# Kernel tuning notes

Hardware: AMD Instinct MI355X
Metric: run time of the kernel (lower is better)

Reference implementation:

```python
import jax, jax.numpy as jnp
import numpy as np

X, Y, Z, E, K, ITERS = 128, 128, 8, 64, 3, 3
XYZ = X * Y * Z
IMG_H, IMG_W = 384, 1280
FH, FW = 96, 320  # img_feat spatial size
LN_EPS = 1e-5
GRAD_SCALE = 0.1


def _homo_grid():
    # get_coordinates: meshgrid(arange(x), -arange(y), arange(z)), then append ones
    xs = (np.arange(X) * 0.8 + 0.0).astype(np.float32)
    ys = (-(np.arange(Y) * 0.8 - 51.2)).astype(np.float32)
    zs = (np.arange(Z) * 0.5 - 2.5).astype(np.float32)
    gx, gy, gz = np.meshgrid(xs, ys, zs, indexing='ij')
    g = np.stack([gx, gy, gz, np.ones_like(gx)], axis=-1)  # (X,Y,Z,4)
    return jnp.asarray(g)


def _grid_sample(img, grid):
    # F.grid_sample: bilinear, padding_mode='zeros', align_corners=False
    # img: (B,C,H,W), grid: (B,N,K,2) xy in [-1,1] -> out (B,C,N,K)
    B, C, H, W = img.shape
    x = ((grid[..., 0] + 1.0) * W - 1.0) * 0.5
    y = ((grid[..., 1] + 1.0) * H - 1.0) * 0.5
    x0 = jnp.floor(x); y0 = jnp.floor(y)
    x1 = x0 + 1.0; y1 = y0 + 1.0
    wx1 = x - x0; wx0 = 1.0 - wx1
    wy1 = y - y0; wy0 = 1.0 - wy1
    flat = img.reshape(B, C, H * W)

    def gather(xi, yi):
        valid = (xi >= 0) & (xi < W) & (yi >= 0) & (yi < H)  # (B,N,K)
        xi_c = jnp.clip(xi, 0, W - 1).astype(jnp.int32)
        yi_c = jnp.clip(yi, 0, H - 1).astype(jnp.int32)
        idx = yi_c * W + xi_c  # (B,N,K)
        g = jnp.take_along_axis(flat, idx.reshape(B, 1, -1), axis=2)
        g = g.reshape(B, C, idx.shape[1], idx.shape[2])
        return g * valid[:, None].astype(img.dtype)

    out = (gather(x0, y0) * (wx0 * wy0)[:, None]
           + gather(x1, y0) * (wx1 * wy0)[:, None]
           + gather(x0, y1) * (wx0 * wy1)[:, None]
           + gather(x1, y1) * (wx1 * wy1)[:, None])
    return out


def setup_inputs() -> dict:
    key = jax.random.key(0)
    ks = jax.random.split(key, 8)
    # realistic extrinsic (velo->cam) and intrinsic so projections land in-image
    T_velo2cam = jnp.array([[[0., -1., 0., 0.],
                             [0., 0., -1., -0.3],
                             [1., 0., 0., 0.5]]], dtype=jnp.float32)
    intrinsic = jnp.array([[[700., 0., 640.],
                            [0., 700., 192.],
                            [0., 0., 1.]]], dtype=jnp.float32)
    img_feat = jax.random.normal(ks[0], (1, E, FH, FW), jnp.float32)
    bev_embedding = 0.1 * jax.random.normal(ks[1], (X, Y, Z, E), jnp.float32)
    W_off = 0.02 * jax.random.normal(ks[2], (ITERS, E, 2 * K), jnp.float32)
    b_off = 0.02 * jax.random.normal(ks[3], (ITERS, 2 * K), jnp.float32)
    s_off = jnp.full((ITERS,), 0.1, jnp.float32)  # Scale(0.1)
    W_w = 0.02 * jax.random.normal(ks[4], (ITERS, E, K), jnp.float32)
    b_w = jnp.zeros((ITERS, K), jnp.float32)
    W_l = (E ** -0.5) * jax.random.normal(ks[5], (ITERS, E, E), jnp.float32)
    b_l = jnp.zeros((ITERS, E), jnp.float32)
    ln_g = jnp.ones((ITERS, E), jnp.float32)
    ln_b = jnp.zeros((ITERS, E), jnp.float32)
    return dict(T_velo2cam=T_velo2cam, intrinsic=intrinsic, img_feat=img_feat,
                bev_embedding=bev_embedding, W_off=W_off, b_off=b_off, s_off=s_off,
                W_w=W_w, b_w=b_w, W_l=W_l, b_l=b_l, ln_g=ln_g, ln_b=ln_b)


def reference(T_velo2cam, intrinsic, img_feat, bev_embedding,
              W_off, b_off, s_off, W_w, b_w, W_l, b_l, ln_g, ln_b):
    homo = _homo_grid()  # (X,Y,Z,4)
    T = jnp.einsum('bij,bjk->bik', intrinsic, T_velo2cam)  # (B,3,4)
    pts = jnp.einsum('bij,xyzj->bxyzi', T, homo)  # (B,X,Y,Z,3)
    uv = pts[..., 0:2] / pts[..., 2:3]
    half = jnp.array([IMG_W / 2.0, IMG_H / 2.0], pts.dtype)
    coord = (uv / half - 1.0).reshape(1, XYZ, 1, 2)  # (B,XYZ,1,2)
    bev = bev_embedding.reshape(1, XYZ, 1, E)
    for i in range(ITERS):
        off = (bev @ W_off[i] + b_off[i]) * s_off[i]  # Linear -> Scale
        # GradientScale(0.1): identity fwd, grad*0.1 bwd
        off = GRAD_SCALE * off + jax.lax.stop_gradient((1.0 - GRAD_SCALE) * off)
        off = off.reshape(1, XYZ, K, 2)
        w = jax.nn.softmax(bev @ W_w[i] + b_w[i], axis=-1)[:, :, 0, :]  # (1,XYZ,K)
        feat = _grid_sample(img_feat, coord + off)  # (1,E,XYZ,K)
        feat = jnp.sum(feat * w[:, None], axis=-1)  # (1,E,XYZ)
        bev = bev + jnp.transpose(feat, (0, 2, 1))[:, :, None, :]  # (1,XYZ,1,E)
        # LinearLNDropout (dropout inactive in eval)
        h = bev @ W_l[i] + b_l[i]
        mu = jnp.mean(h, axis=-1, keepdims=True)
        var = jnp.mean((h - mu) ** 2, axis=-1, keepdims=True)
        h = (h - mu) * jax.lax.rsqrt(var + LN_EPS) * ln_g[i] + ln_b[i]
        bev = bev + h
    bev = bev.reshape(1, X, Y, Z, E)
    return jnp.transpose(bev, (0, 4, 2, 1, 3)).mean(-1)  # (B,E,Y,X)
```

## Files before the change

### kernel.cpp

```cpp
#include <hip/hip_runtime.h>
#include <math.h>

#define XD 128
#define YD 128
#define ZD 8
#define ED 64
#define KD 3
#define NITER 3
#define FHD 96
#define FWD 320
#define HALF_W 640.0f
#define HALF_H 192.0f

#define ASTRIDE 80
#define DSTR 28
#define HSTR 68

#define WAVE_LDS 4352

typedef __attribute__((ext_vector_type(8))) short short8;
typedef __attribute__((ext_vector_type(4))) float f32x4;
typedef float          __attribute__((may_alias)) fal;
typedef unsigned short __attribute__((may_alias)) usal;

__device__ __forceinline__ unsigned short f2bf(float f) {
    unsigned u = __float_as_uint(f);
    u += 0x7fff + ((u >> 16) & 1);
    return (unsigned short)(u >> 16);
}

__device__ __forceinline__ float rdlane_f(float v, int s) {
    return __int_as_float(__builtin_amdgcn_readlane(__float_as_int(v), s));
}

__device__ __forceinline__ float rowsum16(float v) {
    v += __int_as_float(__builtin_amdgcn_update_dpp(0, __float_as_int(v), 0x121, 0xf, 0xf, true));
    v += __int_as_float(__builtin_amdgcn_update_dpp(0, __float_as_int(v), 0x122, 0xf, 0xf, true));
    v += __int_as_float(__builtin_amdgcn_update_dpp(0, __float_as_int(v), 0x124, 0xf, 0xf, true));
    v += __int_as_float(__builtin_amdgcn_update_dpp(0, __float_as_int(v), 0x128, 0xf, 0xf, true));
    return v;
}

__global__ __launch_bounds__(256) void k_prep(const float* __restrict__ img,
                                              float* __restrict__ outHWC,
                                              const float* __restrict__ W_off,
                                              const float* __restrict__ W_w,
                                              const float* __restrict__ W_l,
                                              unsigned short* __restrict__ W9f,
                                              unsigned short* __restrict__ Wlf) {
    if (blockIdx.x < (FHD * FWD) / 64) {
        __shared__ float tile[64][65];
        const int hw0 = blockIdx.x * 64;
        const int lane = threadIdx.x & 63;
        const int r = threadIdx.x >> 6;
#pragma unroll
        for (int i = 0; i < 16; ++i) {
            int e = r + 4 * i;
            tile[e][lane] = img[e * (FHD * FWD) + hw0 + lane];
        }
        __syncthreads();
#pragma unroll
        for (int i = 0; i < 16; ++i) {
            int row = r + 4 * i;
            outHWC[(hw0 + row) * 64 + lane] = tile[lane][row];
        }
    } else {
        int idx = (blockIdx.x - (FHD * FWD) / 64) * 256 + threadIdx.x;
        if (idx < 3 * 4 * 2 * 64) {
            int lane = idx & 63, s = (idx >> 6) & 1, t = (idx >> 7) & 3, i = idx >> 9;
            int n = t * 16 + (lane & 15), quad = lane >> 4;
#pragma unroll
            for (int jj = 0; jj < 8; ++jj) {
                int ep = s * 32 + quad * 8 + jj;
                Wlf[idx * 8 + jj] = f2bf(W_l[(i * ED + ep) * ED + n]);
            }
        } else if (idx < 3 * 4 * 2 * 64 + 3 * 2 * 64) {
            int k = idx - 3 * 4 * 2 * 64;
            int lane = k & 63, s = (k >> 6) & 1, i = k >> 7;
            int n = lane & 15, quad = lane >> 4;
#pragma unroll
            for (int jj = 0; jj < 8; ++jj) {
                int ep = s * 32 + quad * 8 + jj;
                float v = 0.0f;
                if (n < 6) v = W_off[(i * ED + ep) * 6 + n];
                else if (n < 9) v = W_w[(i * ED + ep) * 3 + (n - 6)];
                W9f[k * 8 + jj] = f2bf(v);
            }
        } else if (idx < 3 * 4 * 2 * 64 + 3 * 2 * 64 + 64) {
            outHWC[FHD * FWD * 64 + (idx - (3 * 4 * 2 * 64 + 3 * 2 * 64))] = 0.0f;
        }
    }
}

__global__ __launch_bounds__(256, 4) void k_main(
    const float* __restrict__ Tv,
    const float* __restrict__ intr,
    const float* __restrict__ imgHWC,
    const float* __restrict__ bev_in,
    const unsigned short* __restrict__ W9f,
    const unsigned short* __restrict__ Wlf,
    const float* __restrict__ b_off,
    const float* __restrict__ s_off,
    const float* __restrict__ b_w,
    const float* __restrict__ b_l,
    const float* __restrict__ ln_g,
    const float* __restrict__ ln_b,
    float* __restrict__ tmp)
{
    __shared__ __align__(16) char smem[4 * WAVE_LDS];

    const int lane = threadIdx.x & 63;
    const int wv = threadIdx.x >> 6;
    const int wid2 = __builtin_amdgcn_readfirstlane(blockIdx.x * 4 + wv);
    const int m16 = lane & 15;
    const int quad = lane >> 4;

    char* base = smem + wv * WAVE_LDS;
    usal* Ab = (usal*)base;
    fal*  Db = (fal*)base;
    fal*  Hb = (fal*)base;

    const char* imgB = (const char*)imgHWC;

    float T[12];
#pragma unroll
    for (int r = 0; r < 3; ++r)
#pragma unroll
        for (int c = 0; c < 4; ++c)
            T[r * 4 + c] = intr[r * 3 + 0] * Tv[0 * 4 + c] +
                           intr[r * 3 + 1] * Tv[1 * 4 + c] +
                           intr[r * 3 + 2] * Tv[2 * 4 + c];

    const int sm = min(lane / 3, 15);
    const int sk = lane - (lane / 3) * 3;

    float cxd, cyd;
    {
        int p = sm >> 3, z = sm & 7;
        int q = 2 * wid2 + p;
        int x = q & (XD - 1);
        int y = q >> 7;
        float gx = x * 0.8f;
        float gy = 51.2f - y * 0.8f;
        float gz = z * 0.5f - 2.5f;
        float p0 = T[0] * gx + T[1] * gy + T[2] * gz + T[3];
        float p1 = T[4] * gx + T[5] * gy + T[6] * gz + T[7];
        float p2 = T[8] * gx + T[9] * gy + T[10] * gz + T[11];
        cxd = (p0 / p2) / HALF_W - 1.0f;
        cyd = (p1 / p2) / HALF_H - 1.0f;
    }

    float bev[16];
#pragma unroll
    for (int p = 0; p < 2; ++p) {
        int q = 2 * wid2 + p;
        int x = q & (XD - 1);
        int y = q >> 7;
        int pbase = (((x << 7) | y) << 9);
#pragma unroll
        for (int z = 0; z < ZD; ++z)
            bev[p * 8 + z] = bev_in[pbase + z * ED + lane];
    }

    for (int i = 0; i < NITER; ++i) {
#pragma unroll
        for (int m = 0; m < 16; ++m) Ab[m * ASTRIDE + lane] = f2bf(bev[m]);

        short8 wb0 = *(const short8*)(W9f + ((i * 2 + 0) * 64 + lane) * 8);
        short8 wb1 = *(const short8*)(W9f + ((i * 2 + 1) * 64 + lane) * 8);
        short8 a0 = *(const short8*)(Ab + m16 * ASTRIDE + quad * 8);
        short8 a1 = *(const short8*)(Ab + m16 * ASTRIDE + 32 + quad * 8);
        f32x4 dlog = {0.0f, 0.0f, 0.0f, 0.0f};
        dlog = __builtin_amdgcn_mfma_f32_16x16x32_bf16(a0, wb0, dlog, 0, 0, 0);
        dlog = __builtin_amdgcn_mfma_f32_16x16x32_bf16(a1, wb1, dlog, 0, 0, 0);
#pragma unroll
        for (int r = 0; r < 4; ++r) Db[(quad * 4 + r) * DSTR + m16] = dlog[r];

        const float so = s_off[i];
        const float bo0 = b_off[i * 6 + 0], bo1 = b_off[i * 6 + 1], bo2 = b_off[i * 6 + 2];
        const float bo3 = b_off[i * 6 + 3], bo4 = b_off[i * 6 + 4], bo5 = b_off[i * 6 + 5];
        const float bw0 = b_w[i * 3 + 0], bw1 = b_w[i * 3 + 1], bw2 = b_w[i * 3 + 2];

        int rowA, rowB;
        float dw0, dw1, dw2, dw3;
        {
            const fal* Dm = Db + sm * DSTR;
            f32x4 qa = *(const f32x4*)(Dm);
            f32x4 qb = *(const f32x4*)(Dm + 4);
            float l8 = Dm[8];

            float ox0 = (qa[0] + bo0) * so, oy0 = (qa[1] + bo1) * so;
            float ox1 = (qa[2] + bo2) * so, oy1 = (qa[3] + bo3) * so;
            float ox2 = (qb[0] + bo4) * so, oy2 = (qb[1] + bo5) * so;
            float l0 = qb[2] + bw0, l1 = qb[3] + bw1, l2 = l8 + bw2;
            float mx = fmaxf(fmaxf(l0, l1), l2);
            float e0 = __expf(l0 - mx), e1 = __expf(l1 - mx), e2 = __expf(l2 - mx);
            float inv = 1.0f / (e0 + e1 + e2);
            float wk0 = e0 * inv, wk1 = e1 * inv, wk2 = e2 * inv;

            float wkk = (sk == 0) ? wk0 : ((sk == 1) ? wk1 : wk2);
            float ox  = (sk == 0) ? ox0 : ((sk == 1) ? ox1 : ox2);
            float oy  = (sk == 0) ? oy0 : ((sk == 1) ? oy1 : oy2);

            float gxx = cxd + ox, gyy = cyd + oy;
            float px = ((gxx + 1.0f) * (float)FWD - 1.0f) * 0.5f;
            float py = ((gyy + 1.0f) * (float)FHD - 1.0f) * 0.5f;
            float x0f = floorf(px), y0f = floorf(py);
            float fx = px - x0f, fy = py - y0f;
            int ix0 = (int)x0f, iy0 = (int)y0f;
            int iy1 = iy0 + 1;

            int cb = min(max(ix0, 0), FWD - 1);
            float wA = (ix0 >= 0 && ix0 < FWD) ? (1.0f - fx)
                                               : ((ix0 == -1) ? fx : 0.0f);
            float wB = (ix0 >= 0 && ix0 + 1 < FWD) ? fx : 0.0f;

            int rb0 = min(max(iy0, 0), FHD - 1);
            int rb1 = min(max(iy1, 0), FHD - 1);
            float wy0v = (iy0 >= 0 && iy0 < FHD) ? (1.0f - fy) : 0.0f;
            float wy1v = (iy1 >= 0 && iy1 < FHD) ? fy : 0.0f;

            rowA = rb0 * FWD + cb;
            rowB = rb1 * FWD + cb;
            dw0 = wkk * wA * wy0v;
            dw1 = wkk * wB * wy0v;
            dw2 = wkk * wA * wy1v;
            dw3 = wkk * wB * wy1v;
        }

        float b2[16];
#pragma unroll
        for (int m = 0; m < 16; ++m) {
            float feat = 0.0f;
#pragma unroll
            for (int k = 0; k < KD; ++k) {
                const int s = m * 3 + k;
                int offA = __builtin_amdgcn_readlane(rowA, s);
                int offB = __builtin_amdgcn_readlane(rowB, s);
                float w0 = rdlane_f(dw0, s);
                float w1 = rdlane_f(dw1, s);
                float w2 = rdlane_f(dw2, s);
                float w3 = rdlane_f(dw3, s);
                const fal* pA = (const fal*)(imgB + ((size_t)(unsigned)offA << 8)) + lane;
                const fal* pB = (const fal*)(imgB + ((size_t)(unsigned)offB << 8)) + lane;
                float vA0 = pA[0], vA1 = pA[64];
                float vB0 = pB[0], vB1 = pB[64];
                feat = fmaf(w0, vA0, feat);
                feat = fmaf(w1, vA1, feat);
                feat = fmaf(w2, vB0, feat);
                feat = fmaf(w3, vB1, feat);
            }
            b2[m] = bev[m] + feat;
        }

#pragma unroll
        for (int m = 0; m < 16; ++m) Ab[m * ASTRIDE + lane] = f2bf(b2[m]);
        short8 a0b = *(const short8*)(Ab + m16 * ASTRIDE + quad * 8);
        short8 a1b = *(const short8*)(Ab + m16 * ASTRIDE + 32 + quad * 8);
        f32x4 accs[4];
#pragma unroll
        for (int t = 0; t < 4; ++t) {
            float bb = b_l[i * ED + t * 16 + m16];
            f32x4 acc = {bb, bb, bb, bb};
            short8 w0 = *(const short8*)(Wlf + (((i * 4 + t) * 2 + 0) * 64 + lane) * 8);
            short8 w1 = *(const short8*)(Wlf + (((i * 4 + t) * 2 + 1) * 64 + lane) * 8);
            acc = __builtin_amdgcn_mfma_f32_16x16x32_bf16(a0b, w0, acc, 0, 0, 0);
            acc = __builtin_amdgcn_mfma_f32_16x16x32_bf16(a1b, w1, acc, 0, 0, 0);
            accs[t] = acc;
        }

        float s1[4], s2[4];
#pragma unroll
        for (int r = 0; r < 4; ++r) {
            s1[r] = accs[0][r] + accs[1][r] + accs[2][r] + accs[3][r];
            s2[r] = accs[0][r] * accs[0][r];
            s2[r] = fmaf(accs[1][r], accs[1][r], s2[r]);
            s2[r] = fmaf(accs[2][r], accs[2][r], s2[r]);
            s2[r] = fmaf(accs[3][r], accs[3][r], s2[r]);
            s1[r] = rowsum16(s1[r]);
            s2[r] = rowsum16(s2[r]);
        }
        float gt[4], bt[4];
#pragma unroll
        for (int t = 0; t < 4; ++t) {
            gt[t] = ln_g[i * ED + t * 16 + m16];
            bt[t] = ln_b[i * ED + t * 16 + m16];
        }
#pragma unroll
        for (int r = 0; r < 4; ++r) {
            float mu = s1[r] * (1.0f / 64.0f);
            float var = fmaxf(s2[r] * (1.0f / 64.0f) - mu * mu, 0.0f);
            float rs = rsqrtf(var + 1e-5f);
            int row = quad * 4 + r;
#pragma unroll
            for (int t = 0; t < 4; ++t) {
                float hn = (accs[t][r] - mu) * rs * gt[t] + bt[t];
                Hb[row * HSTR + t * 16 + m16] = hn;
            }
        }
#pragma unroll
        for (int m = 0; m < 16; ++m) bev[m] = b2[m] + Hb[m * HSTR + lane];
    }

#pragma unroll
    for (int p = 0; p < 2; ++p) {
        float s = 0.0f;
#pragma unroll
        for (int z = 0; z < ZD; ++z) s += bev[p * 8 + z];
        tmp[(2 * wid2 + p) * ED + lane] = s * 0.125f;
    }
}

__global__ __launch_bounds__(256) void k_transpose(const float* __restrict__ tmp,
                                                   float* __restrict__ out) {
    __shared__ float tile[64][65];
    const int p0 = blockIdx.x * 64;
    const int lane = threadIdx.x & 63;
    const int r = threadIdx.x >> 6;
#pragma unroll
    for (int i = 0; i < 16; ++i) {
        int row = r + 4 * i;
        tile[row][lane] = tmp[(p0 + row) * ED + lane];
    }
    __syncthreads();
#pragma unroll
    for (int i = 0; i < 16; ++i) {
        int erow = r + 4 * i;
        out[erow * (YD * XD) + p0 + lane] = tile[lane][erow];
    }
}

extern "C" void kernel_launch(void* const* d_in, const int* in_sizes, int n_in,
                              void* d_out, int out_size, void* d_ws, size_t ws_size,
                              hipStream_t stream) {
    const float* Tv      = (const float*)d_in[0];
    const float* intr    = (const float*)d_in[1];
    const float* img     = (const float*)d_in[2];
    const float* bev_in  = (const float*)d_in[3];
    const float* W_off   = (const float*)d_in[4];
    const float* b_off   = (const float*)d_in[5];
    const float* s_off   = (const float*)d_in[6];
    const float* W_w     = (const float*)d_in[7];
    const float* b_w     = (const float*)d_in[8];
    const float* W_l     = (const float*)d_in[9];
    const float* b_l     = (const float*)d_in[10];
    const float* ln_g    = (const float*)d_in[11];
    const float* ln_b    = (const float*)d_in[12];
    float* out = (float*)d_out;

    char* ws = (char*)d_ws;
    float* imgHWC = (float*)ws;
    float* tmp = (float*)(ws + 7864576);
    unsigned short* W9f = (unsigned short*)(ws + 7864576 + 4194304);
    unsigned short* Wlf = (unsigned short*)(ws + 7864576 + 4194304 + 6144);

    k_prep<<<(FHD * FWD) / 64 + 8, 256, 0, stream>>>(img, imgHWC, W_off, W_w, W_l,
                                                     W9f, Wlf);
    k_main<<<(XD * YD / 2) / 4, 256, 0, stream>>>(Tv, intr, imgHWC, bev_in,
                                                  W9f, Wlf, b_off, s_off, b_w,
                                                  b_l, ln_g, ln_b, tmp);
    k_transpose<<<(YD * XD) / 64, 256, 0, stream>>>(tmp, out);
}
```

Measured before the change: 164.4 us.

## Pack image features as bf16 horizontal pairs to halve gather loads

```diff
diff --git a/kernel.cpp b/kernel.cpp
--- a/kernel.cpp
+++ b/kernel.cpp
@@ -21,6 +21,7 @@
 typedef __attribute__((ext_vector_type(8))) short short8;
 typedef __attribute__((ext_vector_type(4))) float f32x4;
 typedef float          __attribute__((may_alias)) fal;
+typedef unsigned       __attribute__((may_alias)) ual;
 typedef unsigned short __attribute__((may_alias)) usal;
 
 __device__ __forceinline__ unsigned short f2bf(float f) {
@@ -42,7 +43,7 @@
 }
 
 __global__ __launch_bounds__(256) void k_prep(const float* __restrict__ img,
-                                              float* __restrict__ outHWC,
+                                              unsigned* __restrict__ imgP,
                                               const float* __restrict__ W_off,
                                               const float* __restrict__ W_w,
                                               const float* __restrict__ W_l,
@@ -59,10 +60,19 @@
             tile[e][lane] = img[e * (FHD * FWD) + hw0 + lane];
         }
         __syncthreads();
+        const bool edge_block = ((hw0 % FWD) == FWD - 64);
 #pragma unroll
         for (int i = 0; i < 16; ++i) {
             int row = r + 4 * i;
-            outHWC[(hw0 + row) * 64 + lane] = tile[lane][row];
+            float v1 = tile[lane][row];
+            float v2;
+            if (row < 63) {
+                v2 = tile[lane][row + 1];
+            } else {
+                v2 = edge_block ? 0.0f : img[lane * (FHD * FWD) + hw0 + 64];
+            }
+            imgP[(hw0 + row) * 64 + lane] =
+                (unsigned)f2bf(v1) | ((unsigned)f2bf(v2) << 16);
         }
     } else {
         int idx = (blockIdx.x - (FHD * FWD) / 64) * 256 + threadIdx.x;
@@ -86,8 +96,6 @@
                 else if (n < 9) v = W_w[(i * ED + ep) * 3 + (n - 6)];
                 W9f[k * 8 + jj] = f2bf(v);
             }
-        } else if (idx < 3 * 4 * 2 * 64 + 3 * 2 * 64 + 64) {
-            outHWC[FHD * FWD * 64 + (idx - (3 * 4 * 2 * 64 + 3 * 2 * 64))] = 0.0f;
         }
     }
 }
@@ -95,7 +103,7 @@
 __global__ __launch_bounds__(256, 4) void k_main(
     const float* __restrict__ Tv,
     const float* __restrict__ intr,
-    const float* __restrict__ imgHWC,
+    const unsigned* __restrict__ imgP,
     const float* __restrict__ bev_in,
     const unsigned short* __restrict__ W9f,
     const unsigned short* __restrict__ Wlf,
@@ -120,7 +128,7 @@
     fal*  Db = (fal*)base;
     fal*  Hb = (fal*)base;
 
-    const char* imgB = (const char*)imgHWC;
+    const char* imgB = (const char*)imgP;
 
     float T[12];
 #pragma unroll
@@ -231,7 +239,7 @@
         float b2[16];
 #pragma unroll
         for (int m = 0; m < 16; ++m) {
-            float feat = 0.0f;
+            float fA0 = 0.0f, fA1 = 0.0f, fB0 = 0.0f, fB1 = 0.0f;
 #pragma unroll
             for (int k = 0; k < KD; ++k) {
                 const int s = m * 3 + k;
@@ -241,16 +249,19 @@
                 float w1 = rdlane_f(dw1, s);
                 float w2 = rdlane_f(dw2, s);
                 float w3 = rdlane_f(dw3, s);
-                const fal* pA = (const fal*)(imgB + ((size_t)(unsigned)offA << 8)) + lane;
-                const fal* pB = (const fal*)(imgB + ((size_t)(unsigned)offB << 8)) + lane;
-                float vA0 = pA[0], vA1 = pA[64];
-                float vB0 = pB[0], vB1 = pB[64];
-                feat = fmaf(w0, vA0, feat);
-                feat = fmaf(w1, vA1, feat);
-                feat = fmaf(w2, vB0, feat);
-                feat = fmaf(w3, vB1, feat);
-            }
-            b2[m] = bev[m] + feat;
+                const ual* pA = (const ual*)(imgB + ((size_t)(unsigned)offA << 8)) + lane;
+                const ual* pB = (const ual*)(imgB + ((size_t)(unsigned)offB << 8)) + lane;
+                unsigned uA = *pA, uB = *pB;
+                float vA0 = __int_as_float((int)(uA << 16));
+                float vA1 = __int_as_float((int)(uA & 0xffff0000u));
+                float vB0 = __int_as_float((int)(uB << 16));
+                float vB1 = __int_as_float((int)(uB & 0xffff0000u));
+                fA0 = fmaf(w0, vA0, fA0);
+                fA1 = fmaf(w1, vA1, fA1);
+                fB0 = fmaf(w2, vB0, fB0);
+                fB1 = fmaf(w3, vB1, fB1);
+            }
+            b2[m] = bev[m] + ((fA0 + fA1) + (fB0 + fB1));
         }
 
 #pragma unroll
@@ -349,14 +360,14 @@
     float* out = (float*)d_out;
 
     char* ws = (char*)d_ws;
-    float* imgHWC = (float*)ws;
-    float* tmp = (float*)(ws + 7864576);
-    unsigned short* W9f = (unsigned short*)(ws + 7864576 + 4194304);
-    unsigned short* Wlf = (unsigned short*)(ws + 7864576 + 4194304 + 6144);
-
-    k_prep<<<(FHD * FWD) / 64 + 8, 256, 0, stream>>>(img, imgHWC, W_off, W_w, W_l,
+    unsigned* imgP = (unsigned*)ws;
+    float* tmp = (float*)(ws + 7864320);
+    unsigned short* W9f = (unsigned short*)(ws + 7864320 + 4194304);
+    unsigned short* Wlf = (unsigned short*)(ws + 7864320 + 4194304 + 6144);
+
+    k_prep<<<(FHD * FWD) / 64 + 8, 256, 0, stream>>>(img, imgP, W_off, W_w, W_l,
                                                      W9f, Wlf);
-    k_main<<<(XD * YD / 2) / 4, 256, 0, stream>>>(Tv, intr, imgHWC, bev_in,
+    k_main<<<(XD * YD / 2) / 4, 256, 0, stream>>>(Tv, intr, imgP, bev_in,
                                                   W9f, Wlf, b_off, s_off, b_w,
                                                   b_l, ln_g, ln_b, tmp);
     k_transpose<<<(YD * XD) / 64, 256, 0, stream>>>(tmp, out);
```

Result: no change. 161.6 us (-1.7%).
